# Optimization experiments

Hardware: AMD Instinct MI355X
Metric: run time of the kernel (lower is better)

Reference implementation:

```python
import jax, jax.numpy as jnp
import numpy as np

D_MODEL = 1024
NHEAD = 8
DPH = D_MODEL // NHEAD
DFF = 2048
EPS = 1e-5


def _layernorm(x, w, b):
    mu = jnp.mean(x, axis=-1, keepdims=True)
    var = jnp.mean((x - mu) ** 2, axis=-1, keepdims=True)
    return (x - mu) / jnp.sqrt(var + EPS) * w + b


def setup_inputs() -> dict:
    key = jax.random.key(0)
    ks = jax.random.split(key, 8)
    B, L = 8, 2048
    x = jax.random.normal(ks[0], (B, L, D_MODEL), dtype=jnp.float32)
    # HeadWiseLinear: per-head weight (nhead, dph, 4*dph), bias (nhead, 4*dph)
    ih_w = jax.random.normal(ks[1], (NHEAD, DPH, 4 * DPH), dtype=jnp.float32) * (1.0 / np.sqrt(DPH))
    # forget-gate bias init: linspace(3,6,d_model) in the f slot (second chunk), zeros elsewhere
    init_vals = jnp.linspace(3.0, 6.0, D_MODEL, dtype=jnp.float32).reshape(NHEAD, 1, DPH)
    init_vals = jnp.pad(init_vals, ((0, 0), (1, 2), (0, 0)))  # rows: i, f, z, o
    ih_b = init_vals.reshape(NHEAD, 4 * DPH)
    # linear_hh: Linear(dph, 4*dph, bias=False), stored as (dph, 4*dph) (x @ W)
    hh_w = jax.random.normal(ks[2], (DPH, 4 * DPH), dtype=jnp.float32) * (1.0 / np.sqrt(DPH))
    ln1_w = jnp.ones((D_MODEL,), jnp.float32); ln1_b = jnp.zeros((D_MODEL,), jnp.float32)
    ln2_w = jnp.ones((D_MODEL,), jnp.float32); ln2_b = jnp.zeros((D_MODEL,), jnp.float32)
    hn_w = jnp.ones((DPH,), jnp.float32); hn_b = jnp.zeros((DPH,), jnp.float32)
    ff_w1 = jax.random.normal(ks[3], (D_MODEL, 2 * DFF), dtype=jnp.float32) * (1.0 / np.sqrt(D_MODEL))
    ff_b1 = jnp.zeros((2 * DFF,), jnp.float32)
    ff_w2 = jax.random.normal(ks[4], (DFF, D_MODEL), dtype=jnp.float32) * (1.0 / np.sqrt(DFF))
    ff_b2 = jnp.zeros((D_MODEL,), jnp.float32)
    return dict(x=x, ih_w=ih_w, ih_b=ih_b, hh_w=hh_w, ln1_w=ln1_w, ln1_b=ln1_b,
                hn_w=hn_w, hn_b=hn_b, ln2_w=ln2_w, ln2_b=ln2_b,
                ff_w1=ff_w1, ff_b1=ff_b1, ff_w2=ff_w2, ff_b2=ff_b2)


def _slstm_core(x, ih_w, ih_b, hh_w, hn_w, hn_b):
    B, L, D = x.shape
    xh = x.reshape(B, L, NHEAD, DPH)
    # headwise input projection: (B,L,H,4*dph)
    proj = jnp.einsum('blhd,hdf->blhf', xh, ih_w) + ih_b
    proj = jnp.transpose(proj, (1, 0, 2, 3))  # (L,B,H,4*dph)

    h0 = jnp.zeros((B, NHEAD, DPH), x.dtype)
    c0 = jnp.zeros_like(h0)
    m0 = jnp.full_like(h0, -jnp.inf)  # stabilizer; matches scalar-0 first-step semantics
    n0 = jnp.zeros_like(h0)

    def step(carry, p_t):
        h, c, m, n = carry
        p = p_t + jnp.einsum('bhd,df->bhf', h, hh_w)
        i, f, z, o = jnp.split(p, 4, axis=-1)
        z = jnp.tanh(z)
        o = jax.nn.sigmoid(o)
        f = jax.nn.log_sigmoid(f) + m
        m_new = jnp.maximum(f, i)
        i_s = jnp.exp(i - m_new)
        f_s = jnp.exp(f - m_new)
        c = f_s * c + i_s * z
        n = f_s * n + i_s
        h = o * (c / n)
        return (h, c, m_new, n), h

    (h, c, _, _), out = jax.lax.scan(step, (h0, c0, m0, n0), proj)
    out = jnp.transpose(out, (1, 0, 2, 3))  # (B,L,H,dph)
    out = _layernorm(out, hn_w, hn_b)
    return out.reshape(B, L, D), (h, c)


def reference(x, ih_w, ih_b, hh_w, ln1_w, ln1_b, hn_w, hn_b, ln2_w, ln2_b,
              ff_w1, ff_b1, ff_w2, ff_b2):
    core_out, _ = _slstm_core(_layernorm(x, ln1_w, ln1_b), ih_w, ih_b, hh_w, hn_w, hn_b)
    y = core_out + x
    z = _layernorm(y, ln2_w, ln2_b)
    x12 = z @ ff_w1 + ff_b1
    x1, x2 = jnp.split(x12, 2, axis=-1)
    ff = (x1 * jax.nn.gelu(x2, approximate=False)) @ ff_w2 + ff_b2
    return ff + y
```

## Files before the change

kernel.cpp:

```cpp
#include <hip/hip_runtime.h>
#include <math.h>


#define D_MODEL 1024
#define NHEAD   8
#define DPH     128
#define DFF     2048
#define BATCH   8
#define SEQ     2048
#define NROWS   (BATCH * SEQ)
#define CHUNK_L 256
#define TGRP    16
#define NGRP    (CHUNK_L / TGRP)
#define ROWCH   8192
#define LN_EPS  1e-5f

typedef __attribute__((ext_vector_type(8))) short short8;
typedef __attribute__((ext_vector_type(4))) float f32x4;
typedef __attribute__((ext_vector_type(2))) _Float16 h2f;
typedef __attribute__((ext_vector_type(8))) _Float16 h8f;
union H8U { h8f v; h2f p[4]; };

#if __has_builtin(__builtin_amdgcn_fdot2)
#define DOT2(a, b, c) __builtin_amdgcn_fdot2((a), (b), (c), false)
#else
__device__ __forceinline__ float DOT2(h2f a, h2f b, float c) {
  return c + (float)a.x * (float)b.x + (float)a.y * (float)b.y;
}
#endif

#if __has_builtin(__builtin_amdgcn_rcpf)
#define FRCP(x) __builtin_amdgcn_rcpf(x)
#else
#define FRCP(x) (1.0f / (x))
#endif

__device__ __forceinline__ float qxor1(float v) {
#if __has_builtin(__builtin_amdgcn_update_dpp)
  union { float f; int i; } u; u.f = v;
  u.i = __builtin_amdgcn_update_dpp(u.i, u.i, 0xB1, 0xf, 0xf, true);
  return u.f;
#else
  return __shfl_xor(v, 1, 64);
#endif
}
__device__ __forceinline__ float qxor2(float v) {
#if __has_builtin(__builtin_amdgcn_update_dpp)
  union { float f; int i; } u; u.f = v;
  u.i = __builtin_amdgcn_update_dpp(u.i, u.i, 0x4E, 0xf, 0xf, true);
  return u.f;
#else
  return __shfl_xor(v, 2, 64);
#endif
}

__device__ __forceinline__ void gll16(const float* src, float* lds_base, int lane) {
#if __has_builtin(__builtin_amdgcn_global_load_lds)
  __builtin_amdgcn_global_load_lds(
      (const __attribute__((address_space(1))) unsigned int*)src,
      (__attribute__((address_space(3))) unsigned int*)lds_base, 16, 0, 0);
#else
  *(float4*)((char*)lds_base + lane * 16) = *(const float4*)src;
#endif
}

__device__ __forceinline__ float gelu_exact(float x) {
  return 0.5f * x * (1.0f + erff(x * 0.70710678118654752440f));
}

__device__ __forceinline__ unsigned short f2bf(float f) {
  union { float f; unsigned int u; } v; v.f = f;
  unsigned int r = v.u + 0x7fffu + ((v.u >> 16) & 1u);
  return (unsigned short)(r >> 16);
}

__device__ __forceinline__ float gate_step(float iv, float fv, float zraw, float oraw,
                                           float& c, float& nrm, float& m) {
  const float zv = 1.0f - 2.0f * FRCP(__expf(2.0f * zraw) + 1.0f);
  const float ov = FRCP(1.0f + __expf(-oraw));
  const float lf = fminf(fv, 0.0f) - __logf(1.0f + __expf(-fabsf(fv)));
  const float ft = lf + m;
  const float mn = fmaxf(ft, iv);
  const float is = __expf(iv - mn);
  const float fs = __expf(ft - mn);
  c = fs * c + is * zv;
  nrm = fs * nrm + is;
  m = mn;
  return ov * c * FRCP(nrm);
}

__global__ __launch_bounds__(256) void ln_stats_kernel(
    const float* __restrict__ in, float* __restrict__ mu_out,
    float* __restrict__ rs_out) {
  const int row = blockIdx.x, tid = threadIdx.x;
  const float4 v = ((const float4*)(in + (size_t)row * D_MODEL))[tid];
  float s  = v.x + v.y + v.z + v.w;
  float s2 = v.x*v.x + v.y*v.y + v.z*v.z + v.w*v.w;
  #pragma unroll
  for (int m = 1; m < 64; m <<= 1) { s += __shfl_xor(s, m, 64); s2 += __shfl_xor(s2, m, 64); }
  __shared__ float sa[4], sb[4];
  if ((tid & 63) == 0) { sa[tid >> 6] = s; sb[tid >> 6] = s2; }
  __syncthreads();
  if (tid == 0) {
    const float S  = sa[0] + sa[1] + sa[2] + sa[3];
    const float S2 = sb[0] + sb[1] + sb[2] + sb[3];
    const float mu = S * (1.0f / D_MODEL);
    const float var = S2 * (1.0f / D_MODEL) - mu * mu;
    mu_out[row] = mu;
    rs_out[row] = rsqrtf(var + LN_EPS);
  }
}

__global__ __launch_bounds__(256) void cvt_w(
    const float* __restrict__ src, short* __restrict__ dst, int K, int N) {
  __shared__ float tile[64][68];
  const int n0 = blockIdx.x * 64;
  const int k0 = blockIdx.y * 64;
  const int tid = threadIdx.x;
  #pragma unroll
  for (int i = 0; i < 16; ++i) {
    const int e = i * 256 + tid;
    const int kk = e >> 6, nn = e & 63;
    tile[kk][nn] = src[(size_t)(k0 + kk) * N + n0 + nn];
  }
  __syncthreads();
  #pragma unroll
  for (int i = 0; i < 2; ++i) {
    const int e = i * 256 + tid;
    const int nn = e >> 3, kc = (e & 7) * 8;
    short8 s;
    #pragma unroll
    for (int j = 0; j < 8; ++j) s[j] = (short)f2bf(tile[kc + j][nn]);
    *(short8*)(dst + (size_t)(n0 + nn) * K + k0 + kc) = s;
  }
}

__global__ __launch_bounds__(256) void cvt_hh(
    const float* __restrict__ hhw, h2f* __restrict__ hh2) {
  const int idx = blockIdx.x * 256 + threadIdx.x;
  const int k2 = idx >> 9, j = idx & 511;
  h2f v;
  v.x = (_Float16)hhw[(size_t)(2 * k2) * 512 + j];
  v.y = (_Float16)hhw[(size_t)(2 * k2 + 1) * 512 + j];
  hh2[idx] = v;
}

__global__ __launch_bounds__(256) void proj_gemm(
    const float* __restrict__ x, const float* __restrict__ mu1,
    const float* __restrict__ rs1, const float* __restrict__ ln1w,
    const float* __restrict__ ln1b, const float* __restrict__ ihw,
    const float* __restrict__ ihb, float* __restrict__ proj, int l0) {
  __shared__ __align__(16) float As[64][68];
  __shared__ __align__(16) float Bs[64][128];
  const int h  = blockIdx.z;
  const int qb = blockIdx.y;
  const int n0 = qb * 128;
  const int m0 = blockIdx.x * 64;
  const int tid = threadIdx.x;
  const int tm = (tid >> 5) << 3;
  const int tn = (tid & 31) << 2;
  float acc[8][4] = {};
  const float* Bb = ihw + (size_t)h * DPH * 512;
  for (int k0 = 0; k0 < DPH; k0 += 64) {
    #pragma unroll
    for (int i = 0; i < 4; ++i) {
      int idx = tid + i * 256;
      int r = idx >> 4, kk = (idx & 15) << 2;
      const int rowm = m0 + r;
      const int l = l0 + (rowm >> 3), b = rowm & 7;
      const int grow = b * SEQ + l;
      const float4 v = *(const float4*)(x + (size_t)grow * D_MODEL + h * DPH + k0 + kk);
      const float mu = mu1[grow], rs = rs1[grow];
      const float4 wv = *(const float4*)(ln1w + h * DPH + k0 + kk);
      const float4 bv = *(const float4*)(ln1b + h * DPH + k0 + kk);
      float4 o;
      o.x = (v.x - mu) * rs * wv.x + bv.x;
      o.y = (v.y - mu) * rs * wv.y + bv.y;
      o.z = (v.z - mu) * rs * wv.z + bv.z;
      o.w = (v.w - mu) * rs * wv.w + bv.w;
      *(float4*)&As[r][kk] = o;
    }
    #pragma unroll
    for (int i = 0; i < 8; ++i) {
      int idx = tid + i * 256;
      int kk = idx >> 5, nn = (idx & 31) << 2;
      *(float4*)&Bs[kk][nn] = *(const float4*)(Bb + (size_t)(k0 + kk) * 512 + n0 + nn);
    }
    __syncthreads();
    #pragma unroll 4
    for (int kk = 0; kk < 64; ++kk) {
      float a[8];
      #pragma unroll
      for (int i = 0; i < 8; ++i) a[i] = As[tm + i][kk];
      const float4 bv = *(const float4*)&Bs[kk][tn];
      #pragma unroll
      for (int i = 0; i < 8; ++i) {
        acc[i][0] += a[i] * bv.x; acc[i][1] += a[i] * bv.y;
        acc[i][2] += a[i] * bv.z; acc[i][3] += a[i] * bv.w;
      }
    }
    __syncthreads();
  }
  const float4 bias = *(const float4*)(ihb + h * 512 + n0 + tn);
  const int pos = n0 + ((tn + 8 * qb) & 127);
  #pragma unroll
  for (int i = 0; i < 8; ++i) {
    const int rowm = m0 + tm + i;
    float4 o;
    o.x = acc[i][0] + bias.x; o.y = acc[i][1] + bias.y;
    o.z = acc[i][2] + bias.z; o.w = acc[i][3] + bias.w;
    *(float4*)(proj + ((size_t)rowm * NHEAD + h) * 512 + pos) = o;
  }
}

__global__ __launch_bounds__(512, 1) void scan_chunk(
    const float* __restrict__ proj, const h2f* __restrict__ hh2,
    float* __restrict__ state, float* __restrict__ hout, int l0) {
  const int bh = blockIdx.x, b = bh >> 3, h = bh & 7;
  const int tid = threadIdx.x;
  const int l = tid & 63, w = tid >> 6;
  const int q = l & 3, p = l >> 2;
  const int ch = 16 * w + p;
  const int pvoff = q * 128 + ((ch + 8 * q) & 127);
  __shared__ __align__(16) _Float16 h16[2][128];
  __shared__ __align__(16) float pbuf[2][TGRP][512];
  __shared__ __align__(16) float hstage[2][TGRP][128];

  h2f w2[4][16];
  #pragma unroll
  for (int j = 0; j < 4; ++j)
    #pragma unroll
    for (int kk = 0; kk < 16; ++kk)
      w2[j][kk] = hh2[(size_t)(16 * q + kk) * 512 + j * 128 + ch];

  float c, nrm, m;
  if (l0 == 0) {
    c = 0.0f; nrm = 0.0f; m = -1e30f;
    if (q == 0) h16[0][ch] = (_Float16)0.0f;
  } else {
    c   = state[bh * 128 + ch];
    nrm = state[8192  + bh * 128 + ch];
    m   = state[16384 + bh * 128 + ch];
    if (q == 0) h16[0][ch] = (_Float16)state[24576 + bh * 128 + ch];
  }

  const float* pbase = proj + (size_t)bh * 512;

  #define STAGE(NB, GR)                                                        \
    {                                                                          \
      _Pragma("unroll")                                                        \
      for (int i = 0; i < 4; ++i) {                                            \
        const int hr = i * 8 + w;                                              \
        const float* src = pbase + (size_t)((GR) * TGRP + (hr >> 1)) * 32768   \
                           + (hr & 1) * 256 + l * 4;                           \
        float* dst = &pbuf[NB][0][0] + hr * 256;                               \
        gll16(src, dst, l);                                                    \
      }                                                                        \
    }

  STAGE(0, 0)
  asm volatile("s_waitcnt vmcnt(0)" ::: "memory");
  __syncthreads();

  float hv = 0.0f;
  for (int grp = 0; grp < NGRP; ++grp) {
    const int gb = grp & 1;
    if (grp + 1 < NGRP) STAGE(gb ^ 1, grp + 1)
    #pragma unroll
    for (int tl = 0; tl < TGRP; ++tl) {
      const int cur = tl & 1;
      float pa0 = 0.0f, pa1 = 0.0f, pa2 = 0.0f, pa3 = 0.0f;
      {
        const h8f* hp = (const h8f*)&h16[cur][q * 32];
        #pragma unroll
        for (int i = 0; i < 4; ++i) {
          H8U u; u.v = hp[i];
          #pragma unroll
          for (int e = 0; e < 4; ++e) {
            const int kk = i * 4 + e;
            pa0 = DOT2(u.p[e], w2[0][kk], pa0);
            pa1 = DOT2(u.p[e], w2[1][kk], pa1);
            pa2 = DOT2(u.p[e], w2[2][kk], pa2);
            pa3 = DOT2(u.p[e], w2[3][kk], pa3);
          }
        }
      }
      const float pv = pbuf[gb][tl][pvoff];
      pa0 += (q == 0) ? pv : 0.0f;
      pa1 += (q == 1) ? pv : 0.0f;
      pa2 += (q == 2) ? pv : 0.0f;
      pa3 += (q == 3) ? pv : 0.0f;
      pa0 += qxor1(pa0); pa1 += qxor1(pa1); pa2 += qxor1(pa2); pa3 += qxor1(pa3);
      pa0 += qxor2(pa0); pa1 += qxor2(pa1); pa2 += qxor2(pa2); pa3 += qxor2(pa3);
      hv = gate_step(pa0, pa1, pa2, pa3, c, nrm, m);
      if (q == 0) {
        h16[cur ^ 1][ch] = (_Float16)hv;
        hstage[gb][tl][ch] = hv;
      }
      __syncthreads();
    }
    {
      const int s = tid >> 5, c8 = (tid & 31) << 2;
      const float4 v0 = *(const float4*)&hstage[gb][s][c8];
      *(float4*)(hout + ((size_t)(b * SEQ + l0 + grp * TGRP + s)) * D_MODEL
                 + h * DPH + c8) = v0;
    }
  }

  if (q == 0) {
    state[bh * 128 + ch]          = c;
    state[8192  + bh * 128 + ch]  = nrm;
    state[16384 + bh * 128 + ch]  = m;
    state[24576 + bh * 128 + ch]  = hv;
  }
  #undef STAGE
}

__global__ __launch_bounds__(256) void post_kernel(
    float* __restrict__ yio, const float* __restrict__ x,
    const float* __restrict__ hnw, const float* __restrict__ hnb,
    float* __restrict__ mu2, float* __restrict__ rs2) {
  const int row = blockIdx.x, tid = threadIdx.x;
  const float4 hv = ((const float4*)(yio + (size_t)row * D_MODEL))[tid];
  float s  = hv.x + hv.y + hv.z + hv.w;
  float s2 = hv.x*hv.x + hv.y*hv.y + hv.z*hv.z + hv.w*hv.w;
  #pragma unroll
  for (int mm = 1; mm < 32; mm <<= 1) {
    s  += __shfl_xor(s,  mm, 32);
    s2 += __shfl_xor(s2, mm, 32);
  }
  const float mu = s * (1.0f / DPH);
  const float var = s2 * (1.0f / DPH) - mu * mu;
  const float rstd = rsqrtf(var + LN_EPS);
  const int dq = tid & 31;
  const float4 w4 = ((const float4*)hnw)[dq];
  const float4 b4 = ((const float4*)hnb)[dq];
  const float4 xv = ((const float4*)(x + (size_t)row * D_MODEL))[tid];
  float4 yv;
  yv.x = (hv.x - mu) * rstd * w4.x + b4.x + xv.x;
  yv.y = (hv.y - mu) * rstd * w4.y + b4.y + xv.y;
  yv.z = (hv.z - mu) * rstd * w4.z + b4.z + xv.z;
  yv.w = (hv.w - mu) * rstd * w4.w + b4.w + xv.w;
  ((float4*)(yio + (size_t)row * D_MODEL))[tid] = yv;
  float t1 = yv.x + yv.y + yv.z + yv.w;
  float t2 = yv.x*yv.x + yv.y*yv.y + yv.z*yv.z + yv.w*yv.w;
  #pragma unroll
  for (int mm = 1; mm < 64; mm <<= 1) {
    t1 += __shfl_xor(t1, mm, 64);
    t2 += __shfl_xor(t2, mm, 64);
  }
  __shared__ float sa[4], sb[4];
  if ((tid & 63) == 0) { sa[tid >> 6] = t1; sb[tid >> 6] = t2; }
  __syncthreads();
  if (tid == 0) {
    const float S  = sa[0] + sa[1] + sa[2] + sa[3];
    const float S2 = sb[0] + sb[1] + sb[2] + sb[3];
    const float m2 = S * (1.0f / D_MODEL);
    const float v2 = S2 * (1.0f / D_MODEL) - m2 * m2;
    mu2[row] = m2;
    rs2[row] = rsqrtf(v2 + LN_EPS);
  }
}

__global__ __launch_bounds__(256) void ff1_gemm(
    const float* __restrict__ y, const float* __restrict__ mu2,
    const float* __restrict__ rs2, const float* __restrict__ ln2w,
    const float* __restrict__ ln2b, const short* __restrict__ w1b,
    const float* __restrict__ b1, short* __restrict__ g, int row0) {
  __shared__ short As[128 * 64];
  __shared__ short Bs1[128 * 64];
  __shared__ short Bs2[128 * 64];
  const int tid = threadIdx.x;
  const int m0 = blockIdx.x * 128;
  const int n0 = blockIdx.y * 128;
  const int lane = tid & 63;
  const int wid = tid >> 6, wr = wid >> 1, wc = wid & 1;
  f32x4 acc1[4][4], acc2[4][4];
  #pragma unroll
  for (int i = 0; i < 4; ++i)
    #pragma unroll
    for (int j = 0; j < 4; ++j) { acc1[i][j] = (f32x4)0.0f; acc2[i][j] = (f32x4)0.0f; }
  for (int k0 = 0; k0 < D_MODEL; k0 += 64) {
    #pragma unroll
    for (int i = 0; i < 4; ++i) {
      const int cidx = tid + i * 256;
      const int r = cidx >> 3, c8 = cidx & 7;
      const int grow = row0 + m0 + r;
      const float* src = y + (size_t)grow * D_MODEL + k0 + c8 * 8;
      const float4 v0 = *(const float4*)src;
      const float4 v1 = *(const float4*)(src + 4);
      const float mu = mu2[grow], rs = rs2[grow];
      const float4 w0 = *(const float4*)(ln2w + k0 + c8 * 8);
      const float4 w1 = *(const float4*)(ln2w + k0 + c8 * 8 + 4);
      const float4 bb0 = *(const float4*)(ln2b + k0 + c8 * 8);
      const float4 bb1 = *(const float4*)(ln2b + k0 + c8 * 8 + 4);
      short8 s;
      s[0] = (short)f2bf((v0.x - mu) * rs * w0.x + bb0.x);
      s[1] = (short)f2bf((v0.y - mu) * rs * w0.y + bb0.y);
      s[2] = (short)f2bf((v0.z - mu) * rs * w0.z + bb0.z);
      s[3] = (short)f2bf((v0.w - mu) * rs * w0.w + bb0.w);
      s[4] = (short)f2bf((v1.x - mu) * rs * w1.x + bb1.x);
      s[5] = (short)f2bf((v1.y - mu) * rs * w1.y + bb1.y);
      s[6] = (short)f2bf((v1.z - mu) * rs * w1.z + bb1.z);
      s[7] = (short)f2bf((v1.w - mu) * rs * w1.w + bb1.w);
      *(short8*)&As[r * 64 + ((c8 ^ (r & 7)) << 3)] = s;
    }
    #pragma unroll
    for (int i = 0; i < 4; ++i) {
      const int cidx = tid + i * 256;
      const int r = cidx >> 3, c8 = cidx & 7;
      const short8 sv1 = *(const short8*)(w1b + (size_t)(n0 + r) * D_MODEL + k0 + c8 * 8);
      const short8 sv2 = *(const short8*)(w1b + (size_t)(DFF + n0 + r) * D_MODEL + k0 + c8 * 8);
      const int off = r * 64 + ((c8 ^ (r & 7)) << 3);
      *(short8*)&Bs1[off] = sv1;
      *(short8*)&Bs2[off] = sv2;
    }
    __syncthreads();
    #pragma unroll
    for (int ks = 0; ks < 2; ++ks) {
      short8 af[4], b1f[4], b2f[4];
      #pragma unroll
      for (int mf = 0; mf < 4; ++mf) {
        const int row = wr * 64 + mf * 16 + (lane & 15);
        const int c8 = ks * 4 + (lane >> 4);
        af[mf] = *(const short8*)&As[row * 64 + ((c8 ^ (row & 7)) << 3)];
      }
      #pragma unroll
      for (int nf = 0; nf < 4; ++nf) {
        const int row = wc * 64 + nf * 16 + (lane & 15);
        const int c8 = ks * 4 + (lane >> 4);
        const int off = row * 64 + ((c8 ^ (row & 7)) << 3);
        b1f[nf] = *(const short8*)&Bs1[off];
        b2f[nf] = *(const short8*)&Bs2[off];
      }
      #pragma unroll
      for (int mf = 0; mf < 4; ++mf)
        #pragma unroll
        for (int nf = 0; nf < 4; ++nf) {
          acc1[mf][nf] = __builtin_amdgcn_mfma_f32_16x16x32_bf16(af[mf], b1f[nf], acc1[mf][nf], 0, 0, 0);
          acc2[mf][nf] = __builtin_amdgcn_mfma_f32_16x16x32_bf16(af[mf], b2f[nf], acc2[mf][nf], 0, 0, 0);
        }
    }
    __syncthreads();
  }
  #pragma unroll
  for (int nf = 0; nf < 4; ++nf) {
    const int col = n0 + wc * 64 + nf * 16 + (lane & 15);
    const float bx1 = b1[col], bx2 = b1[DFF + col];
    #pragma unroll
    for (int mf = 0; mf < 4; ++mf) {
      const int rbase = m0 + wr * 64 + mf * 16 + ((lane >> 4) << 2);
      #pragma unroll
      for (int rr = 0; rr < 4; ++rr) {
        const float x1 = acc1[mf][nf][rr] + bx1;
        const float x2 = acc2[mf][nf][rr] + bx2;
        g[(size_t)(rbase + rr) * DFF + col] = (short)f2bf(x1 * gelu_exact(x2));
      }
    }
  }
}

__global__ __launch_bounds__(256) void ff2_gemm(
    const short* __restrict__ g, const short* __restrict__ w2b,
    const float* __restrict__ b2, float* __restrict__ out, int row0) {
  __shared__ short As[128 * 64];
  __shared__ short Bs[128 * 64];
  const int tid = threadIdx.x;
  const int m0 = blockIdx.x * 128;
  const int n0 = blockIdx.y * 128;
  const int lane = tid & 63;
  const int wid = tid >> 6, wr = wid >> 1, wc = wid & 1;
  f32x4 acc[4][4];
  #pragma unroll
  for (int i = 0; i < 4; ++i)
    #pragma unroll
    for (int j = 0; j < 4; ++j) acc[i][j] = (f32x4)0.0f;
  for (int k0 = 0; k0 < DFF; k0 += 64) {
    #pragma unroll
    for (int i = 0; i < 4; ++i) {
      const int cidx = tid + i * 256;
      const int r = cidx >> 3, c8 = cidx & 7;
      const int off = r * 64 + ((c8 ^ (r & 7)) << 3);
      *(short8*)&As[off] = *(const short8*)(g + (size_t)(m0 + r) * DFF + k0 + c8 * 8);
      *(short8*)&Bs[off] = *(const short8*)(w2b + (size_t)(n0 + r) * DFF + k0 + c8 * 8);
    }
    __syncthreads();
    #pragma unroll
    for (int ks = 0; ks < 2; ++ks) {
      short8 af[4], bf[4];
      #pragma unroll
      for (int mf = 0; mf < 4; ++mf) {
        const int row = wr * 64 + mf * 16 + (lane & 15);
        const int c8 = ks * 4 + (lane >> 4);
        af[mf] = *(const short8*)&As[row * 64 + ((c8 ^ (row & 7)) << 3)];
      }
      #pragma unroll
      for (int nf = 0; nf < 4; ++nf) {
        const int row = wc * 64 + nf * 16 + (lane & 15);
        const int c8 = ks * 4 + (lane >> 4);
        bf[nf] = *(const short8*)&Bs[row * 64 + ((c8 ^ (row & 7)) << 3)];
      }
      #pragma unroll
      for (int mf = 0; mf < 4; ++mf)
        #pragma unroll
        for (int nf = 0; nf < 4; ++nf)
          acc[mf][nf] = __builtin_amdgcn_mfma_f32_16x16x32_bf16(af[mf], bf[nf], acc[mf][nf], 0, 0, 0);
    }
    __syncthreads();
  }
  #pragma unroll
  for (int nf = 0; nf < 4; ++nf) {
    const int col = n0 + wc * 64 + nf * 16 + (lane & 15);
    const float bias = b2[col];
    #pragma unroll
    for (int mf = 0; mf < 4; ++mf) {
      const int rbase = row0 + m0 + wr * 64 + mf * 16 + ((lane >> 4) << 2);
      #pragma unroll
      for (int rr = 0; rr < 4; ++rr) {
        float* p = out + (size_t)(rbase + rr) * D_MODEL + col;
        *p = acc[mf][nf][rr] + bias + *p;
      }
    }
  }
}

extern "C" void kernel_launch(void* const* d_in, const int* in_sizes, int n_in,
                              void* d_out, int out_size, void* d_ws, size_t ws_size,
                              hipStream_t stream) {
  const float* x    = (const float*)d_in[0];
  const float* ihw  = (const float*)d_in[1];
  const float* ihb  = (const float*)d_in[2];
  const float* hhw  = (const float*)d_in[3];
  const float* ln1w = (const float*)d_in[4];
  const float* ln1b = (const float*)d_in[5];
  const float* hnw  = (const float*)d_in[6];
  const float* hnb  = (const float*)d_in[7];
  const float* ln2w = (const float*)d_in[8];
  const float* ln2b = (const float*)d_in[9];
  const float* ffw1 = (const float*)d_in[10];
  const float* ffb1 = (const float*)d_in[11];
  const float* ffw2 = (const float*)d_in[12];
  const float* ffb2 = (const float*)d_in[13];

  float* ws    = (float*)d_ws;
  float* r0    = ws;
  float* state = ws + 8388608;
  float* mu1   = ws + 8421376;
  float* rs1   = ws + 8437760;
  float* mu2   = ws + 8454144;
  float* rs2   = ws + 8470528;
  short* w1b   = (short*)(ws + 8486912);
  short* w2b   = (short*)(ws + 10584064);
  h2f*   hh2   = (h2f*)(ws + 11632640);
  short* gb    = (short*)r0;
  float* out   = (float*)d_out;

  cvt_w<<<dim3(4096 / 64, 1024 / 64), 256, 0, stream>>>(ffw1, w1b, 1024, 4096);
  cvt_w<<<dim3(1024 / 64, 2048 / 64), 256, 0, stream>>>(ffw2, w2b, 2048, 1024);
  cvt_hh<<<128, 256, 0, stream>>>(hhw, hh2);
  ln_stats_kernel<<<NROWS, 256, 0, stream>>>(x, mu1, rs1);
  for (int cidx = 0; cidx < SEQ / CHUNK_L; ++cidx) {
    const int l0 = cidx * CHUNK_L;
    proj_gemm<<<dim3(CHUNK_L * BATCH / 64, 512 / 128, NHEAD), 256, 0, stream>>>(
        x, mu1, rs1, ln1w, ln1b, ihw, ihb, r0, l0);
    scan_chunk<<<BATCH * NHEAD, 512, 0, stream>>>(r0, hh2, state, out, l0);
  }
  post_kernel<<<NROWS, 256, 0, stream>>>(out, x, hnw, hnb, mu2, rs2);
  for (int rc = 0; rc < NROWS / ROWCH; ++rc) {
    const int row0 = rc * ROWCH;
    ff1_gemm<<<dim3(ROWCH / 128, DFF / 128), 256, 0, stream>>>(
        out, mu2, rs2, ln2w, ln2b, w1b, ffb1, gb, row0);
    ff2_gemm<<<dim3(ROWCH / 128, D_MODEL / 128), 256, 0, stream>>>(
        gb, w2b, ffb2, out, row0);
  }
}
```

Baseline: 2.012 ms.

## Pre-tile FFN operands into swizzled LDS images and load via global_load_lds

```diff
diff --git a/kernel.cpp b/kernel.cpp
--- a/kernel.cpp
+++ b/kernel.cpp
@@ -12,10 +12,11 @@
 #define CHUNK_L 256
 #define TGRP    16
 #define NGRP    (CHUNK_L / TGRP)
-#define ROWCH   8192
+#define ROWCH   4096
 #define LN_EPS  1e-5f
 
 typedef __attribute__((ext_vector_type(8))) short short8;
+typedef __attribute__((ext_vector_type(4))) short short4v;
 typedef __attribute__((ext_vector_type(4))) float f32x4;
 typedef __attribute__((ext_vector_type(2))) _Float16 h2f;
 typedef __attribute__((ext_vector_type(8))) _Float16 h8f;
@@ -54,7 +55,7 @@
 #endif
 }
 
-__device__ __forceinline__ void gll16(const float* src, float* lds_base, int lane) {
+__device__ __forceinline__ void gll16(const void* src, void* lds_base, int lane) {
 #if __has_builtin(__builtin_amdgcn_global_load_lds)
   __builtin_amdgcn_global_load_lds(
       (const __attribute__((address_space(1))) unsigned int*)src,
@@ -72,6 +73,10 @@
   union { float f; unsigned int u; } v; v.f = f;
   unsigned int r = v.u + 0x7fffu + ((v.u >> 16) & 1u);
   return (unsigned short)(r >> 16);
+}
+
+__device__ __forceinline__ int img_off(int r, int k) {
+  return r * 64 + ((((k >> 3) & 7) ^ (r & 7)) << 3) + (k & 7);
 }
 
 __device__ __forceinline__ float gate_step(float iv, float fv, float zraw, float oraw,
@@ -124,6 +129,7 @@
     tile[kk][nn] = src[(size_t)(k0 + kk) * N + n0 + nn];
   }
   __syncthreads();
+  const int ktiles = K >> 6;
   #pragma unroll
   for (int i = 0; i < 2; ++i) {
     const int e = i * 256 + tid;
@@ -131,7 +137,9 @@
     short8 s;
     #pragma unroll
     for (int j = 0; j < 8; ++j) s[j] = (short)f2bf(tile[kc + j][nn]);
-    *(short8*)(dst + (size_t)(n0 + nn) * K + k0 + kc) = s;
+    const int n = n0 + nn;
+    const size_t base = ((size_t)(n >> 7) * ktiles + (k0 >> 6)) * 8192;
+    *(short8*)(dst + base + img_off(n & 127, kc)) = s;
   }
 }
 
@@ -362,58 +370,53 @@
   }
 }
 
-__global__ __launch_bounds__(256) void ff1_gemm(
+__global__ __launch_bounds__(256) void cvt_z(
     const float* __restrict__ y, const float* __restrict__ mu2,
     const float* __restrict__ rs2, const float* __restrict__ ln2w,
-    const float* __restrict__ ln2b, const short* __restrict__ w1b,
-    const float* __restrict__ b1, short* __restrict__ g, int row0) {
+    const float* __restrict__ ln2b, short* __restrict__ zb, int row0) {
+  const int lrow = blockIdx.x, tid = threadIdx.x;
+  const int grow = row0 + lrow;
+  const float4 v = ((const float4*)(y + (size_t)grow * D_MODEL))[tid];
+  const float mu = mu2[grow], rs = rs2[grow];
+  const float4 w4 = ((const float4*)ln2w)[tid];
+  const float4 b4 = ((const float4*)ln2b)[tid];
+  short4v s;
+  s[0] = (short)f2bf((v.x - mu) * rs * w4.x + b4.x);
+  s[1] = (short)f2bf((v.y - mu) * rs * w4.y + b4.y);
+  s[2] = (short)f2bf((v.z - mu) * rs * w4.z + b4.z);
+  s[3] = (short)f2bf((v.w - mu) * rs * w4.w + b4.w);
+  const int k = tid * 4;
+  const size_t base = ((size_t)(lrow >> 7) * 16 + (k >> 6)) * 8192;
+  *(short4v*)(zb + base + img_off(lrow & 127, k & 63)) = s;
+}
+
+__global__ __launch_bounds__(256) void ff1_gemm(
+    const short* __restrict__ zb, const short* __restrict__ w1b,
+    const float* __restrict__ b1, short* __restrict__ g) {
   __shared__ short As[128 * 64];
   __shared__ short Bs1[128 * 64];
   __shared__ short Bs2[128 * 64];
   const int tid = threadIdx.x;
-  const int m0 = blockIdx.x * 128;
-  const int n0 = blockIdx.y * 128;
+  const int mb = blockIdx.x;
+  const int nb = blockIdx.y;
   const int lane = tid & 63;
+  const int w = tid >> 6;
   const int wid = tid >> 6, wr = wid >> 1, wc = wid & 1;
+  const short* at = zb + (size_t)mb * 16 * 8192;
+  const short* b1t = w1b + (size_t)nb * 16 * 8192;
+  const short* b2t = w1b + (size_t)(16 + nb) * 16 * 8192;
   f32x4 acc1[4][4], acc2[4][4];
   #pragma unroll
   for (int i = 0; i < 4; ++i)
     #pragma unroll
     for (int j = 0; j < 4; ++j) { acc1[i][j] = (f32x4)0.0f; acc2[i][j] = (f32x4)0.0f; }
-  for (int k0 = 0; k0 < D_MODEL; k0 += 64) {
+  for (int kb = 0; kb < 16; ++kb) {
     #pragma unroll
     for (int i = 0; i < 4; ++i) {
-      const int cidx = tid + i * 256;
-      const int r = cidx >> 3, c8 = cidx & 7;
-      const int grow = row0 + m0 + r;
-      const float* src = y + (size_t)grow * D_MODEL + k0 + c8 * 8;
-      const float4 v0 = *(const float4*)src;
-      const float4 v1 = *(const float4*)(src + 4);
-      const float mu = mu2[grow], rs = rs2[grow];
-      const float4 w0 = *(const float4*)(ln2w + k0 + c8 * 8);
-      const float4 w1 = *(const float4*)(ln2w + k0 + c8 * 8 + 4);
-      const float4 bb0 = *(const float4*)(ln2b + k0 + c8 * 8);
-      const float4 bb1 = *(const float4*)(ln2b + k0 + c8 * 8 + 4);
-      short8 s;
-      s[0] = (short)f2bf((v0.x - mu) * rs * w0.x + bb0.x);
-      s[1] = (short)f2bf((v0.y - mu) * rs * w0.y + bb0.y);
-      s[2] = (short)f2bf((v0.z - mu) * rs * w0.z + bb0.z);
-      s[3] = (short)f2bf((v0.w - mu) * rs * w0.w + bb0.w);
-      s[4] = (short)f2bf((v1.x - mu) * rs * w1.x + bb1.x);
-      s[5] = (short)f2bf((v1.y - mu) * rs * w1.y + bb1.y);
-      s[6] = (short)f2bf((v1.z - mu) * rs * w1.z + bb1.z);
-      s[7] = (short)f2bf((v1.w - mu) * rs * w1.w + bb1.w);
-      *(short8*)&As[r * 64 + ((c8 ^ (r & 7)) << 3)] = s;
-    }
-    #pragma unroll
-    for (int i = 0; i < 4; ++i) {
-      const int cidx = tid + i * 256;
-      const int r = cidx >> 3, c8 = cidx & 7;
-      const short8 sv1 = *(const short8*)(w1b + (size_t)(n0 + r) * D_MODEL + k0 + c8 * 8);
-      const short8 sv2 = *(const short8*)(w1b + (size_t)(DFF + n0 + r) * D_MODEL + k0 + c8 * 8);
-      const int off = r * 64 + ((c8 ^ (r & 7)) << 3);
-      *(short8*)&Bs1[off] = sv1;
-      *(short8*)&Bs2[off] = sv2;
+      const int off = i * 2048 + w * 512;
+      gll16(at + (size_t)kb * 8192 + off + lane * 8, As + off, lane);
+      gll16(b1t + (size_t)kb * 8192 + off + lane * 8, Bs1 + off, lane);
+      gll16(b2t + (size_t)kb * 8192 + off + lane * 8, Bs2 + off, lane);
     }
     __syncthreads();
     #pragma unroll
@@ -445,16 +448,18 @@
   }
   #pragma unroll
   for (int nf = 0; nf < 4; ++nf) {
-    const int col = n0 + wc * 64 + nf * 16 + (lane & 15);
+    const int col = nb * 128 + wc * 64 + nf * 16 + (lane & 15);
     const float bx1 = b1[col], bx2 = b1[DFF + col];
     #pragma unroll
     for (int mf = 0; mf < 4; ++mf) {
-      const int rbase = m0 + wr * 64 + mf * 16 + ((lane >> 4) << 2);
+      const int rloc = wr * 64 + mf * 16 + ((lane >> 4) << 2);
       #pragma unroll
       for (int rr = 0; rr < 4; ++rr) {
         const float x1 = acc1[mf][nf][rr] + bx1;
         const float x2 = acc2[mf][nf][rr] + bx2;
-        g[(size_t)(rbase + rr) * DFF + col] = (short)f2bf(x1 * gelu_exact(x2));
+        const int r = rloc + rr;
+        const size_t base = ((size_t)mb * 32 + (col >> 6)) * 8192;
+        g[base + img_off(r, col & 63)] = (short)f2bf(x1 * gelu_exact(x2));
       }
     }
   }
@@ -466,23 +471,24 @@
   __shared__ short As[128 * 64];
   __shared__ short Bs[128 * 64];
   const int tid = threadIdx.x;
-  const int m0 = blockIdx.x * 128;
-  const int n0 = blockIdx.y * 128;
+  const int mb = blockIdx.x;
+  const int nb = blockIdx.y;
   const int lane = tid & 63;
+  const int w = tid >> 6;
   const int wid = tid >> 6, wr = wid >> 1, wc = wid & 1;
+  const short* at = g + (size_t)mb * 32 * 8192;
+  const short* bt = w2b + (size_t)nb * 32 * 8192;
   f32x4 acc[4][4];
   #pragma unroll
   for (int i = 0; i < 4; ++i)
     #pragma unroll
     for (int j = 0; j < 4; ++j) acc[i][j] = (f32x4)0.0f;
-  for (int k0 = 0; k0 < DFF; k0 += 64) {
+  for (int kb = 0; kb < 32; ++kb) {
     #pragma unroll
     for (int i = 0; i < 4; ++i) {
-      const int cidx = tid + i * 256;
-      const int r = cidx >> 3, c8 = cidx & 7;
-      const int off = r * 64 + ((c8 ^ (r & 7)) << 3);
-      *(short8*)&As[off] = *(const short8*)(g + (size_t)(m0 + r) * DFF + k0 + c8 * 8);
-      *(short8*)&Bs[off] = *(const short8*)(w2b + (size_t)(n0 + r) * DFF + k0 + c8 * 8);
+      const int off = i * 2048 + w * 512;
+      gll16(at + (size_t)kb * 8192 + off + lane * 8, As + off, lane);
+      gll16(bt + (size_t)kb * 8192 + off + lane * 8, Bs + off, lane);
     }
     __syncthreads();
     #pragma unroll
@@ -510,11 +516,11 @@
   }
   #pragma unroll
   for (int nf = 0; nf < 4; ++nf) {
-    const int col = n0 + wc * 64 + nf * 16 + (lane & 15);
+    const int col = nb * 128 + wc * 64 + nf * 16 + (lane & 15);
     const float bias = b2[col];
     #pragma unroll
     for (int mf = 0; mf < 4; ++mf) {
-      const int rbase = row0 + m0 + wr * 64 + mf * 16 + ((lane >> 4) << 2);
+      const int rbase = row0 + mb * 128 + wr * 64 + mf * 16 + ((lane >> 4) << 2);
       #pragma unroll
       for (int rr = 0; rr < 4; ++rr) {
         float* p = out + (size_t)(rbase + rr) * D_MODEL + col;
@@ -553,6 +559,7 @@
   short* w2b   = (short*)(ws + 10584064);
   h2f*   hh2   = (h2f*)(ws + 11632640);
   short* gb    = (short*)r0;
+  short* zb    = (short*)(ws + 4194304);
   float* out   = (float*)d_out;
 
   cvt_w<<<dim3(4096 / 64, 1024 / 64), 256, 0, stream>>>(ffw1, w1b, 1024, 4096);
@@ -568,8 +575,8 @@
   post_kernel<<<NROWS, 256, 0, stream>>>(out, x, hnw, hnb, mu2, rs2);
   for (int rc = 0; rc < NROWS / ROWCH; ++rc) {
     const int row0 = rc * ROWCH;
-    ff1_gemm<<<dim3(ROWCH / 128, DFF / 128), 256, 0, stream>>>(
-        out, mu2, rs2, ln2w, ln2b, w1b, ffb1, gb, row0);
+    cvt_z<<<ROWCH, 256, 0, stream>>>(out, mu2, rs2, ln2w, ln2b, zb, row0);
+    ff1_gemm<<<dim3(ROWCH / 128, DFF / 128), 256, 0, stream>>>(zb, w1b, ffb1, gb);
     ff2_gemm<<<dim3(ROWCH / 128, D_MODEL / 128), 256, 0, stream>>>(
         gb, w2b, ffb2, out, row0);
   }
```

Result: no change. 2.023 ms (+0.6%).
